# Kernel tuning notes

Measured on AMD Instinct MI355X. Metric: run time of the kernel, lower is better.

Reference implementation:

```python
import jax, jax.numpy as jnp
import numpy as np

K = 64  # init kwarg k
B, D = 4096, 16384


def setup_inputs() -> dict:
    key = jax.random.key(0)
    x = jax.random.normal(key, (B, D), dtype=jnp.float32)
    return {"x": x}


def reference(x):
    # top-k along last dim, then scatter values into a zero tensor (same as
    # torch.topk + zeros_like + scatter_).
    vals, idx = jax.lax.top_k(x, K)            # [B, K], [B, K]
    rows = jnp.arange(x.shape[0])[:, None]     # [B, 1] broadcast against idx
    return jnp.zeros_like(x).at[rows, idx].set(vals)
```

## Files before the change

kernel.cpp:

```cpp
#include <hip/hip_runtime.h>


#define TK_D      16384
#define TK_K      64
#define TK_BLOCK  512
#define TK_NF4    8
#define TK_BINS   2048
#define TK_EQCAP  1024

__device__ __forceinline__ unsigned ord_map(unsigned b) {
    return b ^ ((unsigned)((int)b >> 31) | 0x80000000u);
}

__launch_bounds__(TK_BLOCK, 4)
__global__ void topk_scatter_kernel(const float* __restrict__ x,
                                    float* __restrict__ out) {
    __shared__ __align__(16) unsigned sh_vals[TK_D];
    __shared__ int      sh_hist[TK_BINS];
    __shared__ int      sh_wsum[8];
    __shared__ unsigned sh_prefix;
    __shared__ int      sh_rem;
    __shared__ int      sh_eqn;
    __shared__ int      sh_eqidx[TK_EQCAP];

    const int row  = blockIdx.x;
    const int tid  = threadIdx.x;
    const int lane = tid & 63;
    const int wv   = tid >> 6;

    const float4* __restrict__ xrow = (const float4*)(x + (size_t)row * TK_D);

    #pragma unroll
    for (int i = 0; i < TK_NF4; i++) {
        const int c4 = wv * 64 + i * TK_BLOCK;
        __builtin_amdgcn_global_load_lds(
            (const __attribute__((address_space(1))) void*)(xrow + c4 + lane),
            (__attribute__((address_space(3))) void*)(&sh_vals[4 * c4]),
            16, 0, 0);
    }

    ((int4*)sh_hist)[tid] = int4{0, 0, 0, 0};
    if (tid == 0) { sh_prefix = 0u; sh_rem = TK_K; sh_eqn = 0; }
    __syncthreads();

    const int histshift[3]  = {21, 10, 0};
    const int scopeshift[3] = {0, 21, 10};
    const int nbits[3]      = {11, 11, 10};

    for (int p = 0; p < 3; p++) {
        const unsigned pref = sh_prefix;
        const int      rem  = sh_rem;
        const int      hs   = histshift[p];
        const unsigned msk  = (1u << nbits[p]) - 1u;
        #pragma unroll
        for (int i = 0; i < TK_NF4; i++) {
            uint4 b = ((const uint4*)sh_vals)[tid + i * TK_BLOCK];
            #pragma unroll
            for (int c = 0; c < 4; c++) {
                unsigned u = ord_map(((const unsigned*)&b)[c]);
                bool in_scope = (p == 0) || ((u >> scopeshift[p] >> nbits[0]) == pref);
                in_scope = (p == 0) || ((u >> (hs + nbits[p])) == pref);
                if (in_scope) atomicAdd(&sh_hist[(u >> hs) & msk], 1);
            }
        }
        __syncthreads();

        int h0 = sh_hist[4 * tid + 0], h1 = sh_hist[4 * tid + 1];
        int h2 = sh_hist[4 * tid + 2], h3 = sh_hist[4 * tid + 3];
        int local = h0 + h1 + h2 + h3;
        int suf = local;
        #pragma unroll
        for (int off = 1; off < 64; off <<= 1) {
            int o = __shfl_down(suf, off);
            if (lane + off < 64) suf += o;
        }
        if (lane == 0) sh_wsum[wv] = suf;
        __syncthreads();

        ((int4*)sh_hist)[tid] = int4{0, 0, 0, 0};

        int above = 0;
        #pragma unroll
        for (int w2 = 0; w2 < 8; w2++)
            if (w2 > wv) above += sh_wsum[w2];

        int a3 = above + (suf - local);
        int S3 = a3 + h3, S2 = S3 + h2, S1 = S2 + h1, S0 = S1 + h0;
        int d = -1, ab = 0;
        if      (S3 >= rem && a3 < rem) { d = 4 * tid + 3; ab = a3; }
        else if (S2 >= rem && S3 < rem) { d = 4 * tid + 2; ab = S3; }
        else if (S1 >= rem && S2 < rem) { d = 4 * tid + 1; ab = S2; }
        else if (S0 >= rem && S1 < rem) { d = 4 * tid + 0; ab = S1; }
        if (d >= 0) {
            sh_prefix = (pref << nbits[p]) | (unsigned)d;
            sh_rem    = rem - ab;
        }
        __syncthreads();
    }

    const unsigned T    = sh_prefix;
    const int      need = sh_rem;

    float4* __restrict__ orow = (float4*)(out + (size_t)row * TK_D);
    #pragma unroll
    for (int i = 0; i < TK_NF4; i++) {
        const int c4 = tid + i * TK_BLOCK;
        uint4 b = ((const uint4*)sh_vals)[c4];
        float4 o;
        #pragma unroll
        for (int c = 0; c < 4; c++) {
            unsigned raw = ((const unsigned*)&b)[c];
            unsigned u   = ord_map(raw);
            ((float*)&o)[c] = (u > T) ? __uint_as_float(raw) : 0.0f;
            if (u == T) {
                int pos = atomicAdd(&sh_eqn, 1);
                if (pos < TK_EQCAP) sh_eqidx[pos] = 4 * c4 + c;
            }
        }
        orow[c4] = o;
    }
    __syncthreads();

    const int L = min(sh_eqn, TK_EQCAP);
    for (int i = tid; i < L; i += TK_BLOCK) {
        int col  = sh_eqidx[i];
        int rank = 0;
        for (int j = 0; j < L; j++) rank += (sh_eqidx[j] < col);
        if (rank < need)
            out[(size_t)row * TK_D + col] = __uint_as_float(sh_vals[col]);
    }
}

extern "C" void kernel_launch(void* const* d_in, const int* in_sizes, int n_in,
                              void* d_out, int out_size, void* d_ws, size_t ws_size,
                              hipStream_t stream) {
    const float* x = (const float*)d_in[0];
    float* out = (float*)d_out;
    const int B = in_sizes[0] / TK_D;
    topk_scatter_kernel<<<B, TK_BLOCK, 0, stream>>>(x, out);
}
```

Before: 444.6 us.

## Replace three-pass radix select with one histogram pass plus candidate ranking

Drops the 64KB LDS row buffer and the three-pass 11/11/10-bit radix select. The new kernel builds one 2048-bin histogram on the top bits, finds the boundary bin, then rereads the row from global memory to write the output and collect boundary-bin candidates into LDS. The exact threshold comes from an O(C^2) rank among those candidates. LDS use falls, which raises occupancy (256 threads, launch bound 6), at the cost of reading the row twice. Candidates beyond the 2048-entry cap would be silently dropped, and a crowded boundary bin makes the quadratic ranking expensive.

```diff
diff --git a/kernel.cpp b/kernel.cpp
--- a/kernel.cpp
+++ b/kernel.cpp
@@ -3,25 +3,31 @@
 
 #define TK_D      16384
 #define TK_K      64
-#define TK_BLOCK  512
-#define TK_NF4    8
+#define TK_T      256
+#define TK_C4     16
 #define TK_BINS   2048
-#define TK_EQCAP  1024
+#define TK_BPT    8
+#define TK_CAP    2048
 
 __device__ __forceinline__ unsigned ord_map(unsigned b) {
     return b ^ ((unsigned)((int)b >> 31) | 0x80000000u);
 }
+__device__ __forceinline__ float ord_unmap(unsigned u) {
+    return __uint_as_float(u ^ ((unsigned)((int)(~u) >> 31) | 0x80000000u));
+}
 
-__launch_bounds__(TK_BLOCK, 4)
+__launch_bounds__(TK_T, 6)
 __global__ void topk_scatter_kernel(const float* __restrict__ x,
                                     float* __restrict__ out) {
-    __shared__ __align__(16) unsigned sh_vals[TK_D];
     __shared__ int      sh_hist[TK_BINS];
-    __shared__ int      sh_wsum[8];
-    __shared__ unsigned sh_prefix;
+    __shared__ unsigned sh_cu[TK_CAP];
+    __shared__ int      sh_ci[TK_CAP];
+    __shared__ int      sh_wsum[4];
+    __shared__ unsigned sh_B0;
     __shared__ int      sh_rem;
-    __shared__ int      sh_eqn;
-    __shared__ int      sh_eqidx[TK_EQCAP];
+    __shared__ int      sh_cn;
+    __shared__ unsigned sh_T;
+    __shared__ int      sh_gT;
 
     const int row  = blockIdx.x;
     const int tid  = threadIdx.x;
@@ -29,45 +35,31 @@
     const int wv   = tid >> 6;
 
     const float4* __restrict__ xrow = (const float4*)(x + (size_t)row * TK_D);
+    float4* __restrict__ orow       = (float4*)(out + (size_t)row * TK_D);
+
+    ((int4*)sh_hist)[2 * tid]     = int4{0, 0, 0, 0};
+    ((int4*)sh_hist)[2 * tid + 1] = int4{0, 0, 0, 0};
+    if (tid == 0) sh_cn = 0;
+    __syncthreads();
 
     #pragma unroll
-    for (int i = 0; i < TK_NF4; i++) {
-        const int c4 = wv * 64 + i * TK_BLOCK;
-        __builtin_amdgcn_global_load_lds(
-            (const __attribute__((address_space(1))) void*)(xrow + c4 + lane),
-            (__attribute__((address_space(3))) void*)(&sh_vals[4 * c4]),
-            16, 0, 0);
+    for (int i = 0; i < TK_C4; i++) {
+        float4 v = xrow[tid + i * TK_T];
+        #pragma unroll
+        for (int c = 0; c < 4; c++) {
+            unsigned u = ord_map(__float_as_uint(((const float*)&v)[c]));
+            atomicAdd(&sh_hist[u >> 21], 1);
+        }
     }
-
-    ((int4*)sh_hist)[tid] = int4{0, 0, 0, 0};
-    if (tid == 0) { sh_prefix = 0u; sh_rem = TK_K; sh_eqn = 0; }
     __syncthreads();
 
-    const int histshift[3]  = {21, 10, 0};
-    const int scopeshift[3] = {0, 21, 10};
-    const int nbits[3]      = {11, 11, 10};
-
-    for (int p = 0; p < 3; p++) {
-        const unsigned pref = sh_prefix;
-        const int      rem  = sh_rem;
-        const int      hs   = histshift[p];
-        const unsigned msk  = (1u << nbits[p]) - 1u;
+    {
+        int h[TK_BPT];
         #pragma unroll
-        for (int i = 0; i < TK_NF4; i++) {
-            uint4 b = ((const uint4*)sh_vals)[tid + i * TK_BLOCK];
-            #pragma unroll
-            for (int c = 0; c < 4; c++) {
-                unsigned u = ord_map(((const unsigned*)&b)[c]);
-                bool in_scope = (p == 0) || ((u >> scopeshift[p] >> nbits[0]) == pref);
-                in_scope = (p == 0) || ((u >> (hs + nbits[p])) == pref);
-                if (in_scope) atomicAdd(&sh_hist[(u >> hs) & msk], 1);
-            }
-        }
-        __syncthreads();
-
-        int h0 = sh_hist[4 * tid + 0], h1 = sh_hist[4 * tid + 1];
-        int h2 = sh_hist[4 * tid + 2], h3 = sh_hist[4 * tid + 3];
-        int local = h0 + h1 + h2 + h3;
+        for (int c = 0; c < TK_BPT; c++) h[c] = sh_hist[TK_BPT * tid + c];
+        int local = 0;
+        #pragma unroll
+        for (int c = 0; c < TK_BPT; c++) local += h[c];
         int suf = local;
         #pragma unroll
         for (int off = 1; off < 64; off <<= 1) {
@@ -76,58 +68,71 @@
         }
         if (lane == 0) sh_wsum[wv] = suf;
         __syncthreads();
+        int above = suf - local;
+        #pragma unroll
+        for (int w2 = 0; w2 < 4; w2++)
+            if (w2 > wv) above += sh_wsum[w2];
+        int s_excl = above;
+        #pragma unroll
+        for (int c = TK_BPT - 1; c >= 0; c--) {
+            int S = s_excl + h[c];
+            if (S >= TK_K && s_excl < TK_K) {
+                sh_B0  = (unsigned)(TK_BPT * tid + c);
+                sh_rem = TK_K - s_excl;
+            }
+            s_excl = S;
+        }
+    }
+    __syncthreads();
+    const unsigned B0   = sh_B0;
+    const int      remB = sh_rem;
 
-        ((int4*)sh_hist)[tid] = int4{0, 0, 0, 0};
-
-        int above = 0;
-        #pragma unroll
-        for (int w2 = 0; w2 < 8; w2++)
-            if (w2 > wv) above += sh_wsum[w2];
-
-        int a3 = above + (suf - local);
-        int S3 = a3 + h3, S2 = S3 + h2, S1 = S2 + h1, S0 = S1 + h0;
-        int d = -1, ab = 0;
-        if      (S3 >= rem && a3 < rem) { d = 4 * tid + 3; ab = a3; }
-        else if (S2 >= rem && S3 < rem) { d = 4 * tid + 2; ab = S3; }
-        else if (S1 >= rem && S2 < rem) { d = 4 * tid + 1; ab = S2; }
-        else if (S0 >= rem && S1 < rem) { d = 4 * tid + 0; ab = S1; }
-        if (d >= 0) {
-            sh_prefix = (pref << nbits[p]) | (unsigned)d;
-            sh_rem    = rem - ab;
-        }
-        __syncthreads();
-    }
-
-    const unsigned T    = sh_prefix;
-    const int      need = sh_rem;
-
-    float4* __restrict__ orow = (float4*)(out + (size_t)row * TK_D);
     #pragma unroll
-    for (int i = 0; i < TK_NF4; i++) {
-        const int c4 = tid + i * TK_BLOCK;
-        uint4 b = ((const uint4*)sh_vals)[c4];
+    for (int i = 0; i < TK_C4; i++) {
+        const int c4 = tid + i * TK_T;
+        float4 v = xrow[c4];
         float4 o;
         #pragma unroll
         for (int c = 0; c < 4; c++) {
-            unsigned raw = ((const unsigned*)&b)[c];
-            unsigned u   = ord_map(raw);
-            ((float*)&o)[c] = (u > T) ? __uint_as_float(raw) : 0.0f;
-            if (u == T) {
-                int pos = atomicAdd(&sh_eqn, 1);
-                if (pos < TK_EQCAP) sh_eqidx[pos] = 4 * c4 + c;
+            float    f   = ((const float*)&v)[c];
+            unsigned u   = ord_map(__float_as_uint(f));
+            unsigned bin = u >> 21;
+            ((float*)&o)[c] = (bin > B0) ? f : 0.0f;
+            if (bin == B0) {
+                int pos = atomicAdd(&sh_cn, 1);
+                if (pos < TK_CAP) { sh_cu[pos] = u; sh_ci[pos] = 4 * c4 + c; }
             }
         }
         orow[c4] = o;
     }
     __syncthreads();
 
-    const int L = min(sh_eqn, TK_EQCAP);
-    for (int i = tid; i < L; i += TK_BLOCK) {
-        int col  = sh_eqidx[i];
-        int rank = 0;
-        for (int j = 0; j < L; j++) rank += (sh_eqidx[j] < col);
-        if (rank < need)
-            out[(size_t)row * TK_D + col] = __uint_as_float(sh_vals[col]);
+    const int C = min(sh_cn, TK_CAP);
+    for (int i = tid; i < C; i += TK_T) {
+        unsigned ui = sh_cu[i];
+        int g = 0, e = 0;
+        for (int j = 0; j < C; j++) {
+            unsigned uj = sh_cu[j];
+            g += (uj > ui);
+            e += (uj == ui);
+        }
+        if (g < remB && g + e >= remB) { sh_T = ui; sh_gT = g; }
+    }
+    __syncthreads();
+    const unsigned T    = sh_T;
+    const int      need = remB - sh_gT;
+
+    for (int i = tid; i < C; i += TK_T) {
+        unsigned ui = sh_cu[i];
+        if (ui > T) {
+            out[(size_t)row * TK_D + sh_ci[i]] = ord_unmap(ui);
+        } else if (ui == T) {
+            int ci = sh_ci[i], r = 0;
+            for (int j = 0; j < C; j++)
+                r += (sh_cu[j] == T && sh_ci[j] < ci);
+            if (r < need)
+                out[(size_t)row * TK_D + ci] = ord_unmap(ui);
+        }
     }
 }
 
@@ -137,5 +142,5 @@
     const float* x = (const float*)d_in[0];
     float* out = (float*)d_out;
     const int B = in_sizes[0] / TK_D;
-    topk_scatter_kernel<<<B, TK_BLOCK, 0, stream>>>(x, out);
+    topk_scatter_kernel<<<B, TK_T, 0, stream>>>(x, out);
 }
```

Result: slower. 470.6 us (+5.8%).
